# Kernel optimization log

Measured on AMD Instinct MI355X. Metric: run time of the kernel, lower is better.

The kernel has to match this reference:

```python
import jax, jax.numpy as jnp
import numpy as np
import math

B, S, N, D_IN = 32, 60, 25, 100
GRU, TEMB, SEMB, SEM_IN, CH, OUT, NH = 512, 512, 512, 768, 256, 512, 8


def _ln(x, g, b, eps=1e-5):
    m = jnp.mean(x, axis=-1, keepdims=True)
    v = jnp.mean((x - m) ** 2, axis=-1, keepdims=True)
    return (x - m) * jax.lax.rsqrt(v + eps) * g + b


def _gru_dir(x, w_ih, w_hh, b_ih, b_hh, reverse):
    # x: [BN, S, F]; PyTorch GRU gate order (r, z, n); returns final hidden [BN, H]
    H = w_hh.shape[1]
    gi_all = jnp.einsum('bsf,gf->bsg', x, w_ih) + b_ih  # precompute input-side gates

    def step(h, gi):
        gh = h @ w_hh.T + b_hh
        i_r, i_z, i_n = jnp.split(gi, 3, axis=-1)
        h_r, h_z, h_n = jnp.split(gh, 3, axis=-1)
        r = jax.nn.sigmoid(i_r + h_r)
        z = jax.nn.sigmoid(i_z + h_z)
        n = jnp.tanh(i_n + r * h_n)
        h_new = (1.0 - z) * n + z * h
        return h_new, None

    h0 = jnp.zeros((x.shape[0], H), x.dtype)
    h_last, _ = jax.lax.scan(step, h0, jnp.swapaxes(gi_all, 0, 1), reverse=reverse)
    return h_last


def _forward(x, seq1_w1, seq1_b1, seq1_w2, seq1_b2, ln2_g, ln2_b,
             gru_wih_f, gru_whh_f, gru_bih_f, gru_bhh_f,
             gru_wih_b, gru_whh_b, gru_bih_b, gru_bhh_b,
             ln_g, ln_b, attn_in_w, attn_in_b, fc_ta_w, fc_ta_b,
             ln3_g, ln3_b, semantic_embs, sem_w, sem_b, lnsem_g, lnsem_b,
             att_alpha, dist_adj,
             gcn_w0, gcn_b0, gcn_w1, gcn_b1, gcn_w2, gcn_b2,
             gln1_g, gln1_b, gln2_g, gln2_b,
             enc_ln_g, enc_ln_b, fc_w, fc_b):
    Bx, Sx, Nx, _ = x.shape
    # --- latent_correlation_layer ---
    xr = jnp.transpose(x, (0, 2, 1, 3)).reshape(Bx * Nx, Sx, -1)  # [BN,S,D]
    h = jax.nn.relu(xr @ seq1_w1 + seq1_b1)
    h = jax.nn.relu(h @ seq1_w2 + seq1_b2)  # dropout p=0
    h = _ln(h, ln2_g, ln2_b)  # [BN,S,512]
    hf = _gru_dir(h, gru_wih_f, gru_whh_f, gru_bih_f, gru_bhh_f, False)
    hb = _gru_dir(h, gru_wih_b, gru_whh_b, gru_bih_b, gru_bhh_b, True)
    hn = jnp.concatenate([hf, hb], axis=-1).reshape(Bx, Nx, 2 * GRU)
    hn = _ln(hn, ln_g, ln_b)  # [B,N,2*GRU]
    # multihead self-attention weights (averaged over heads, then over batch)
    hd = (2 * GRU) // NH
    qkv = hn @ attn_in_w.T + attn_in_b
    q, k, _v = jnp.split(qkv, 3, axis=-1)
    q = q.reshape(Bx, Nx, NH, hd)
    k = k.reshape(Bx, Nx, NH, hd)
    scores = jnp.einsum('bihd,bjhd->bhij', q, k) / math.sqrt(hd)
    attention = jax.nn.softmax(scores, axis=-1).mean(axis=1).mean(axis=0)  # [N,N]
    # --- node features ---
    wr = jax.nn.relu(hn @ fc_ta_w + fc_ta_b)
    X = _ln(wr, ln3_g, ln3_b)  # [B,N,TEMB]
    te = _ln(semantic_embs @ sem_w + sem_b, lnsem_g, lnsem_b)  # [N,SEMB]
    X = jnp.concatenate([X, jnp.broadcast_to(te, (Bx,) + te.shape)], axis=-1)  # [B,N,TEMB+SEMB]
    # cosine-similarity embedding attention (same for every batch element)
    en = te / jnp.maximum(jnp.linalg.norm(te, axis=-1, keepdims=True), 1e-8)
    embed_att = en @ en.T  # [N,N]
    attention = (att_alpha * dist_adj + (1.0 - att_alpha) * embed_att) * attention
    # case-amplification mask (detached in the original -> stop_gradient)
    m = jax.lax.stop_gradient(attention)
    m = jnp.maximum(m, 0.0) ** 2.5
    m = m / jnp.max(m)
    mask = (m >= 0.08).astype(x.dtype)
    adj = attention * mask
    # --- GCN block (GCNConv, add_self_loops=False, normalize=False, dense adjacency) ---
    def gcn(Xin, W, b):
        # out[i] = sum_j adj[j,i] * (Xin[j] @ W) + b  (source->target flow)
        return jnp.einsum('ji,bjf->bif', adj, Xin @ W) + b
    Xg = jax.nn.relu(gcn(X, gcn_w0, gcn_b0))
    Xg = jax.nn.relu(_ln(gcn(Xg, gcn_w1, gcn_b1) + Xg, gln1_g, gln1_b))
    Xg = jax.nn.relu(_ln(gcn(Xg, gcn_w2, gcn_b2) + Xg, gln2_g, gln2_b))
    # --- encoder head ---
    Xg = _ln(Xg, enc_ln_g, enc_ln_b)
    X_hat = jax.nn.relu(jnp.concatenate([X, Xg], axis=-1) @ fc_w + fc_b)  # [B,N,OUT]
    return X_hat


def setup_inputs():
    key = jax.random.key(0)
    c = [0]

    def nrm(shape, scale=1.0):
        c[0] += 1
        return (jax.random.normal(jax.random.fold_in(key, c[0]), shape) * scale).astype(jnp.float32)

    z = lambda *s: jnp.zeros(s, jnp.float32)
    o = lambda *s: jnp.ones(s, jnp.float32)
    FDIM = TEMB + SEMB
    d = {
        'x': nrm((B, S, N, D_IN)),
        'seq1_w1': nrm((D_IN, 256), 0.06), 'seq1_b1': z(256),
        'seq1_w2': nrm((256, 512), 0.05), 'seq1_b2': z(512),
        'ln2_g': o(512), 'ln2_b': z(512),
        'gru_wih_f': nrm((3 * GRU, 512), 0.04), 'gru_whh_f': nrm((3 * GRU, GRU), 0.04),
        'gru_bih_f': z(3 * GRU), 'gru_bhh_f': z(3 * GRU),
        'gru_wih_b': nrm((3 * GRU, 512), 0.04), 'gru_whh_b': nrm((3 * GRU, GRU), 0.04),
        'gru_bih_b': z(3 * GRU), 'gru_bhh_b': z(3 * GRU),
        'ln_g': o(2 * GRU), 'ln_b': z(2 * GRU),
        'attn_in_w': nrm((3 * 2 * GRU, 2 * GRU), 0.03), 'attn_in_b': z(3 * 2 * GRU),
        'fc_ta_w': nrm((2 * GRU, TEMB), 0.04), 'fc_ta_b': z(TEMB),
        'ln3_g': o(TEMB), 'ln3_b': z(TEMB),
        'semantic_embs': nrm((N, SEM_IN)),
        'sem_w': nrm((SEM_IN, SEMB), 0.04), 'sem_b': z(SEMB),
        'lnsem_g': o(SEMB), 'lnsem_b': z(SEMB),
        'att_alpha': jnp.float32(0.5),
        'dist_adj': jax.random.uniform(jax.random.fold_in(key, 1000), (N, N), jnp.float32),
        'gcn_w0': nrm((FDIM, CH), 0.04), 'gcn_b0': z(CH),
        'gcn_w1': nrm((CH, CH), 0.06), 'gcn_b1': z(CH),
        'gcn_w2': nrm((CH, CH), 0.06), 'gcn_b2': z(CH),
        'gln1_g': o(CH), 'gln1_b': z(CH),
        'gln2_g': o(CH), 'gln2_b': z(CH),
        'enc_ln_g': o(CH), 'enc_ln_b': z(CH),
        'fc_w': nrm((FDIM + CH, OUT), 0.04), 'fc_b': z(OUT),
    }
    return d


def reference(x, seq1_w1, seq1_b1, seq1_w2, seq1_b2, ln2_g, ln2_b,
              gru_wih_f, gru_whh_f, gru_bih_f, gru_bhh_f,
              gru_wih_b, gru_whh_b, gru_bih_b, gru_bhh_b,
              ln_g, ln_b, attn_in_w, attn_in_b, fc_ta_w, fc_ta_b,
              ln3_g, ln3_b, semantic_embs, sem_w, sem_b, lnsem_g, lnsem_b,
              att_alpha, dist_adj,
              gcn_w0, gcn_b0, gcn_w1, gcn_b1, gcn_w2, gcn_b2,
              gln1_g, gln1_b, gln2_g, gln2_b,
              enc_ln_g, enc_ln_b, fc_w, fc_b):
    return _forward(x, seq1_w1, seq1_b1, seq1_w2, seq1_b2, ln2_g, ln2_b,
                    gru_wih_f, gru_whh_f, gru_bih_f, gru_bhh_f,
                    gru_wih_b, gru_whh_b, gru_bih_b, gru_bhh_b,
                    ln_g, ln_b, attn_in_w, attn_in_b, fc_ta_w, fc_ta_b,
                    ln3_g, ln3_b, semantic_embs, sem_w, sem_b, lnsem_g, lnsem_b,
                    att_alpha, dist_adj,
                    gcn_w0, gcn_b0, gcn_w1, gcn_b1, gcn_w2, gcn_b2,
                    gln1_g, gln1_b, gln2_g, gln2_b,
                    enc_ln_g, enc_ln_b, fc_w, fc_b)
```

## Files before the change

kernel.cpp:

```cpp
#include <hip/hip_runtime.h>
#include <hip/hip_bf16.h>
#include <math.h>

#define BB 32
#define SS 60
#define NN_ 25
#define DIN 100
#define BN 800
#define GRU_H 512
#define FDIM 1024
#define CH 256
#define OUTD 512

typedef unsigned short ushort_t;
typedef unsigned int u32;
typedef unsigned long long u64;
typedef float f32x4 __attribute__((ext_vector_type(4)));
typedef __bf16 bf16x8 __attribute__((ext_vector_type(8)));
typedef short s16x8 __attribute__((ext_vector_type(8)));

static const size_t O_HSEQB = 0;
static const size_t O_WB    = 12288000;
static const size_t O_HF32  = 13860864;
static const size_t O_HRING = 14680064;
static const size_t O_HN    = 15908864;
static const size_t O_QKV   = 16728064;
static const size_t O_SC    = 18366464;
static const size_t O_ADJ   = 18530304;
static const size_t O_WR    = 18530944;
static const size_t O_TEP   = 18940544;
static const size_t O_TE    = 18953344;
static const size_t O_XCAT  = 18966144;
static const size_t O_GTMP  = 19990144;
static const size_t O_XG0   = 20194944;
static const size_t O_XG1   = 20399744;
static const size_t O_XG2   = 20604544;
static const size_t O_W1TB  = 20809344;
static const size_t O_W2TB  = 20825728;
static const size_t O_AWB   = 20891264;
static const size_t O_FTWB  = 21939840;
static const size_t O_SMWB  = 22201984;
static const size_t O_G0WB  = 22398592;
static const size_t O_G1WB  = 22529664;
static const size_t O_G2WB  = 22562432;
static const size_t O_FCWB  = 22595200;
static const size_t O_FLAGS = 22922880;

__device__ __forceinline__ ushort_t f2b(float v)
{
  __hip_bfloat16 b = __float2bfloat16(v);
  return *reinterpret_cast<ushort_t*>(&b);
}

__device__ __forceinline__ float sig_fast(float v)
{
  return 1.f / (1.f + __expf(-v));
}
__device__ __forceinline__ float tanh_fast(float v)
{
  return 1.f - 2.f / (1.f + __expf(2.f * v));
}

__device__ __forceinline__ void block_reduce2(float& s, float& q, float* scratch)
{
  __syncthreads();
  #pragma unroll
  for (int off = 32; off > 0; off >>= 1) {
    s += __shfl_down(s, off);
    q += __shfl_down(q, off);
  }
  int tid = threadIdx.x;
  int w = tid >> 6;
  if ((tid & 63) == 0) { scratch[w * 2] = s; scratch[w * 2 + 1] = q; }
  __syncthreads();
  if (tid == 0) {
    float ss = 0.f, qq = 0.f;
    int nw = blockDim.x >> 6;
    for (int i = 0; i < nw; i++) { ss += scratch[i * 2]; qq += scratch[i * 2 + 1]; }
    scratch[0] = ss; scratch[1] = qq;
  }
  __syncthreads();
  s = scratch[0]; q = scratch[1];
}

__global__ __launch_bounds__(256) void k_cvt_plain_all(
    const float* __restrict__ wih_f, const float* __restrict__ whh_f,
    const float* __restrict__ wih_b, const float* __restrict__ whh_b,
    const float* __restrict__ attn_w,
    ushort_t* __restrict__ wb, ushort_t* __restrict__ awb)
{
  int i = blockIdx.x * 256 + threadIdx.x;
  wb[i]           = f2b(wih_f[i]);
  wb[786432 + i]  = f2b(whh_f[i]);
  wb[1572864 + i] = f2b(wih_b[i]);
  wb[2359296 + i] = f2b(whh_b[i]);
  awb[i]          = f2b(attn_w[i]);
  awb[786432 + i] = f2b(attn_w[786432 + i]);
  int j = 1572864 + i;
  if (j < 2097152) awb[j] = f2b(attn_w[j]);
}

struct TJob {
  const float* src; ushort_t* dst;
  int K, N, KP, base;
};

__global__ __launch_bounds__(256) void k_cvt_t_all(
    TJob j0, TJob j1, TJob j2, TJob j3, TJob j4, TJob j5, TJob j6, TJob j7)
{
  __shared__ float tile[32][33];
  int t = blockIdx.x;
  TJob jb = j0;
  if (t >= j7.base) jb = j7;
  else if (t >= j6.base) jb = j6;
  else if (t >= j5.base) jb = j5;
  else if (t >= j4.base) jb = j4;
  else if (t >= j3.base) jb = j3;
  else if (t >= j2.base) jb = j2;
  else if (t >= j1.base) jb = j1;
  int local = t - jb.base;
  int ktiles = (jb.KP + 31) >> 5;
  int n0 = (local / ktiles) * 32;
  int k0 = (local % ktiles) * 32;
  int tx = threadIdx.x & 31, ty = threadIdx.x >> 5;
  #pragma unroll
  for (int i = 0; i < 4; i++) {
    int k = k0 + ty + i * 8, n = n0 + tx;
    tile[ty + i * 8][tx] = (k < jb.K && n < jb.N) ? jb.src[(size_t)k * jb.N + n] : 0.f;
  }
  __syncthreads();
  #pragma unroll
  for (int i = 0; i < 4; i++) {
    int n = n0 + ty + i * 8, k = k0 + tx;
    if (n < jb.N && k < jb.KP) jb.dst[(size_t)n * jb.KP + k] = f2b(tile[tx][ty + i * 8]);
  }
}

__global__ __launch_bounds__(256, 1) void k_mlp_fused(
    const float* __restrict__ x,
    const ushort_t* __restrict__ w1tb,
    const float* __restrict__ b1,
    const ushort_t* __restrict__ w2tb,
    const float* __restrict__ b2,
    const float* __restrict__ g, const float* __restrict__ be,
    ushort_t* __restrict__ hseqb)
{
  __shared__ __align__(16) ushort_t xb[64][136];
  __shared__ __align__(16) ushort_t Bl[512][40];
  __shared__ __align__(16) ushort_t h1[64][264];
  const int tid = threadIdx.x;
  const int r0 = blockIdx.x * 64;

  {
    int rr = tid >> 2;
    int d0 = (tid & 3) * 32;
    int r = r0 + rr;
    int bn = r / SS, s = r % SS;
    int b = bn / NN_, n = bn % NN_;
    const float* xp = x + (((size_t)b * SS + s) * NN_ + n) * DIN;
    ushort_t tmp[32];
    #pragma unroll
    for (int i = 0; i < 32; i++) {
      int d = d0 + i;
      tmp[i] = (d < DIN) ? f2b(xp[d]) : (ushort_t)0;
    }
    #pragma unroll
    for (int i = 0; i < 4; i++)
      *reinterpret_cast<s16x8*>(&xb[rr][d0 + i * 8]) = *reinterpret_cast<s16x8*>(&tmp[i * 8]);
  }
  const int wid = tid >> 6, l = tid & 63, lr = l & 15, lg = l >> 4;
  const int srow = tid >> 2, skg = (tid & 3) * 8;

  f32x4 acc1[16] = {};
  for (int kc = 0; kc < 4; kc++) {
    __syncthreads();
    #pragma unroll
    for (int i = 0; i < 4; i++) {
      int row = srow + i * 64;
      *reinterpret_cast<s16x8*>(&Bl[row][skg]) =
          *reinterpret_cast<const s16x8*>(w1tb + (size_t)row * 128 + kc * 32 + skg);
    }
    __syncthreads();
    bf16x8 aF = *reinterpret_cast<const bf16x8*>(&xb[wid * 16 + lr][kc * 32 + lg * 8]);
    #pragma unroll
    for (int ni = 0; ni < 16; ni++) {
      bf16x8 bF = *reinterpret_cast<const bf16x8*>(&Bl[ni * 16 + lr][lg * 8]);
      acc1[ni] = __builtin_amdgcn_mfma_f32_16x16x32_bf16(aF, bF, acc1[ni], 0, 0, 0);
    }
  }
  #pragma unroll
  for (int ni = 0; ni < 16; ni++) {
    #pragma unroll
    for (int r = 0; r < 4; r++) {
      int row = wid * 16 + lg * 4 + r;
      int col = ni * 16 + lr;
      h1[row][col] = f2b(fmaxf(acc1[ni][r] + b1[col], 0.f));
    }
  }

  f32x4 acc2[32] = {};
  for (int kc = 0; kc < 8; kc++) {
    __syncthreads();
    #pragma unroll
    for (int i = 0; i < 8; i++) {
      int row = srow + i * 64;
      *reinterpret_cast<s16x8*>(&Bl[row][skg]) =
          *reinterpret_cast<const s16x8*>(w2tb + (size_t)row * 256 + kc * 32 + skg);
    }
    __syncthreads();
    bf16x8 aF = *reinterpret_cast<const bf16x8*>(&h1[wid * 16 + lr][kc * 32 + lg * 8]);
    #pragma unroll
    for (int ni = 0; ni < 32; ni++) {
      bf16x8 bF = *reinterpret_cast<const bf16x8*>(&Bl[ni * 16 + lr][lg * 8]);
      acc2[ni] = __builtin_amdgcn_mfma_f32_16x16x32_bf16(aF, bF, acc2[ni], 0, 0, 0);
    }
  }

  float su[4] = {0.f, 0.f, 0.f, 0.f}, sq[4] = {0.f, 0.f, 0.f, 0.f};
  #pragma unroll
  for (int ni = 0; ni < 32; ni++) {
    float bb = b2[ni * 16 + lr];
    #pragma unroll
    for (int r = 0; r < 4; r++) {
      float v = fmaxf(acc2[ni][r] + bb, 0.f);
      acc2[ni][r] = v;
      su[r] += v; sq[r] += v * v;
    }
  }
  #pragma unroll
  for (int off = 1; off < 16; off <<= 1) {
    #pragma unroll
    for (int r = 0; r < 4; r++) {
      su[r] += __shfl_xor(su[r], off);
      sq[r] += __shfl_xor(sq[r], off);
    }
  }
  #pragma unroll
  for (int r = 0; r < 4; r++) {
    float mean = su[r] * (1.f / 512.f);
    float var = sq[r] * (1.f / 512.f) - mean * mean;
    float rs = rsqrtf(var + 1e-5f);
    int rowg = r0 + wid * 16 + lg * 4 + r;
    ushort_t* outp = hseqb + (size_t)rowg * 512;
    #pragma unroll
    for (int ni = 0; ni < 32; ni++) {
      int col = ni * 16 + lr;
      outp[col] = f2b((acc2[ni][r] - mean) * rs * g[col] + be[col]);
    }
  }
}

__global__ __launch_bounds__(256, 1) void k_gru_persist(
    const ushort_t* __restrict__ hseqb, const ushort_t* __restrict__ wb,
    const float* __restrict__ bih_f, const float* __restrict__ bhh_f,
    const float* __restrict__ bih_b, const float* __restrict__ bhh_b,
    float* __restrict__ hf32, ushort_t* __restrict__ hring,
    int* __restrict__ flags)
{
  __shared__ __align__(16) ushort_t Xs[2][64][40];
  __shared__ __align__(16) ushort_t Ws[2][6][64][40];
  __shared__ __align__(16) ushort_t Hs[64][520];
  __shared__ int s_item;
  ushort_t (*hpack)[64] = reinterpret_cast<ushort_t (*)[64]>(&Xs[0][0][0]);

  const int tid = threadIdx.x;

  int* qcnt = flags + 448;
  if (tid == 0) {
    u32 xcc;
    asm volatile("s_getreg_b32 %0, hwreg(HW_REG_XCC_ID)" : "=s"(xcc));
    xcc &= 7u;
    int idx = __hip_atomic_fetch_add(qcnt + xcc, 1, __ATOMIC_RELAXED,
                                     __HIP_MEMORY_SCOPE_AGENT);
    s_item = (idx << 3) | (int)xcc;
  }
  __syncthreads();
  const int xcd = s_item & 7;
  const int idx = s_item >> 3;
  const int x3 = xcd & 3;
  const int dir = xcd >> 2;
  const int nmt = (x3 == 0) ? 4 : 3;
  if (idx >= nmt * 8) return;
  const int mt = (idx >> 3) * 4 + x3;
  const int jt = idx & 7;
  const int j0g = jt * 64;
  const int m0g = mt * 64;
  const int chain = dir * 13 + mt;
  int* flagp = flags + chain * 16;

  const ushort_t* __restrict__ wih = wb + (size_t)dir * 1572864;
  const ushort_t* __restrict__ whh = wih + 786432;
  const float* __restrict__ bih = dir ? bih_b : bih_f;
  const float* __restrict__ bhh = dir ? bhh_b : bhh_f;
  const size_t dirOff = (size_t)dir * 409600;

  const int srow = tid >> 2;
  const int skg = (tid & 3) * 8;
  const int smg = m0g + srow;
  const int smg_c = (smg < BN) ? smg : 0;

  const ushort_t* pw[6];
  #pragma unroll
  for (int tt = 0; tt < 6; tt++) {
    const ushort_t* src = (tt < 3) ? wih : whh;
    int gate = (tt < 3) ? tt : tt - 3;
    int jglob = gate * 512 + j0g + srow;
    pw[tt] = src + (size_t)jglob * 512 + skg;
  }

  const int wid = tid >> 6;
  const int l = tid & 63;
  const int lr = l & 15;
  const int lg = l >> 4;
  const int mbase = (wid >> 1) * 32;
  const int nbase = (wid & 1) * 32;

  float rbr[2], rbz[2], rbin[2], rbhn[2];
  #pragma unroll
  for (int ni = 0; ni < 2; ni++) {
    int j = j0g + nbase + ni * 16 + lr;
    rbr[ni]  = bih[j] + bhh[j];
    rbz[ni]  = bih[512 + j] + bhh[512 + j];
    rbin[ni] = bih[1024 + j];
    rbhn[ni] = bhh[1024 + j];
  }

  float hpreg[2][2][4] = {};

  for (int t = 0; t < SS; ++t) {
    const int xt = dir ? (SS - 1 - t) : t;
    const ushort_t* __restrict__ hprev = hring + (size_t)(t % 3) * 819200 + dirOff;
    ushort_t* __restrict__ hnew = hring + (size_t)((t + 1) % 3) * 819200 + dirOff;
    const ushort_t* __restrict__ px = hseqb + ((size_t)smg_c * SS + xt) * 512 + skg;

    s16x8 rx = *reinterpret_cast<const s16x8*>(px);
    s16x8 rw[6];
    #pragma unroll
    for (int tt = 0; tt < 6; tt++) rw[tt] = *reinterpret_cast<const s16x8*>(pw[tt]);

    if (t > 0 && tid == 0) {
      while (__hip_atomic_load(flagp, __ATOMIC_RELAXED, __HIP_MEMORY_SCOPE_SYSTEM) < 8 * t) {
        __builtin_amdgcn_s_sleep(2);
      }
    }
    __syncthreads();

    {
      const ushort_t* ph = hprev + (size_t)smg_c * 512 + skg;
      u64 hv[32];
      #pragma unroll
      for (int c = 0; c < 16; c++) {
        hv[2 * c]     = *reinterpret_cast<const volatile u64*>(ph + c * 32);
        hv[2 * c + 1] = *reinterpret_cast<const volatile u64*>(ph + c * 32 + 4);
      }
      #pragma unroll
      for (int c = 0; c < 16; c++) {
        *reinterpret_cast<u64*>(&Hs[srow][c * 32 + skg])     = hv[2 * c];
        *reinterpret_cast<u64*>(&Hs[srow][c * 32 + skg + 4]) = hv[2 * c + 1];
      }
    }
    *reinterpret_cast<s16x8*>(&Xs[0][srow][skg]) = rx;
    #pragma unroll
    for (int tt = 0; tt < 6; tt++) *reinterpret_cast<s16x8*>(&Ws[0][tt][srow][skg]) = rw[tt];
    __syncthreads();

    f32x4 accr[2][2] = {};
    f32x4 accz[2][2] = {};
    f32x4 accin[2][2] = {};
    f32x4 acchn[2][2] = {};

    for (int it = 0; it < 16; ++it) {
      const int cur = it & 1;
      if (it < 15) {
        const int k0 = (it + 1) * 32;
        rx = *reinterpret_cast<const s16x8*>(px + k0);
        #pragma unroll
        for (int tt = 0; tt < 6; tt++) rw[tt] = *reinterpret_cast<const s16x8*>(pw[tt] + k0);
      }

      bf16x8 xA[2], hA[2];
      #pragma unroll
      for (int mi = 0; mi < 2; mi++) {
        xA[mi] = *reinterpret_cast<const bf16x8*>(&Xs[cur][mbase + mi * 16 + lr][lg * 8]);
        hA[mi] = *reinterpret_cast<const bf16x8*>(&Hs[mbase + mi * 16 + lr][it * 32 + lg * 8]);
      }
      #pragma unroll
      for (int ni = 0; ni < 2; ni++) {
        const int wrow = nbase + ni * 16 + lr;
        bf16x8 bWr = *reinterpret_cast<const bf16x8*>(&Ws[cur][0][wrow][lg * 8]);
        bf16x8 bWz = *reinterpret_cast<const bf16x8*>(&Ws[cur][1][wrow][lg * 8]);
        bf16x8 bWn = *reinterpret_cast<const bf16x8*>(&Ws[cur][2][wrow][lg * 8]);
        bf16x8 bVr = *reinterpret_cast<const bf16x8*>(&Ws[cur][3][wrow][lg * 8]);
        bf16x8 bVz = *reinterpret_cast<const bf16x8*>(&Ws[cur][4][wrow][lg * 8]);
        bf16x8 bVn = *reinterpret_cast<const bf16x8*>(&Ws[cur][5][wrow][lg * 8]);
        #pragma unroll
        for (int mi = 0; mi < 2; mi++) {
          accr[mi][ni]  = __builtin_amdgcn_mfma_f32_16x16x32_bf16(xA[mi], bWr, accr[mi][ni], 0, 0, 0);
          accr[mi][ni]  = __builtin_amdgcn_mfma_f32_16x16x32_bf16(hA[mi], bVr, accr[mi][ni], 0, 0, 0);
          accz[mi][ni]  = __builtin_amdgcn_mfma_f32_16x16x32_bf16(xA[mi], bWz, accz[mi][ni], 0, 0, 0);
          accz[mi][ni]  = __builtin_amdgcn_mfma_f32_16x16x32_bf16(hA[mi], bVz, accz[mi][ni], 0, 0, 0);
          accin[mi][ni] = __builtin_amdgcn_mfma_f32_16x16x32_bf16(xA[mi], bWn, accin[mi][ni], 0, 0, 0);
          acchn[mi][ni] = __builtin_amdgcn_mfma_f32_16x16x32_bf16(hA[mi], bVn, acchn[mi][ni], 0, 0, 0);
        }
      }

      if (it < 15) {
        const int nxt = cur ^ 1;
        *reinterpret_cast<s16x8*>(&Xs[nxt][srow][skg]) = rx;
        #pragma unroll
        for (int tt = 0; tt < 6; tt++) *reinterpret_cast<s16x8*>(&Ws[nxt][tt][srow][skg]) = rw[tt];
      }
      __syncthreads();
    }

    #pragma unroll
    for (int mi = 0; mi < 2; mi++) {
      #pragma unroll
      for (int ni = 0; ni < 2; ni++) {
        #pragma unroll
        for (int r = 0; r < 4; r++) {
          float sr = accr[mi][ni][r] + rbr[ni];
          float sz = accz[mi][ni][r] + rbz[ni];
          float rg = sig_fast(sr);
          float zg = sig_fast(sz);
          float ng = tanh_fast(accin[mi][ni][r] + rbin[ni] + rg * (acchn[mi][ni][r] + rbhn[ni]));
          hpreg[mi][ni][r] = (1.f - zg) * ng + zg * hpreg[mi][ni][r];
        }
      }
    }

    if (t < SS - 1) {
      #pragma unroll
      for (int mi = 0; mi < 2; mi++)
        #pragma unroll
        for (int ni = 0; ni < 2; ni++)
          #pragma unroll
          for (int r = 0; r < 4; r++)
            hpack[mbase + mi * 16 + lg * 4 + r][nbase + ni * 16 + lr] = f2b(hpreg[mi][ni][r]);
      __syncthreads();
      {
        int row = tid >> 2;
        int gm = m0g + row;
        if (gm < BN) {
          ushort_t* dst = hnew + (size_t)gm * 512 + j0g + (tid & 3) * 16;
          *reinterpret_cast<s16x8*>(dst) =
              *reinterpret_cast<s16x8*>(&hpack[row][(tid & 3) * 16]);
          *reinterpret_cast<s16x8*>(dst + 8) =
              *reinterpret_cast<s16x8*>(&hpack[row][(tid & 3) * 16 + 8]);
        }
      }
      __syncthreads();
      if (tid == 0)
        __hip_atomic_fetch_add(flagp, 1, __ATOMIC_RELAXED, __HIP_MEMORY_SCOPE_SYSTEM);
    } else {
      float* hfin = hf32 + dirOff;
      #pragma unroll
      for (int mi = 0; mi < 2; mi++) {
        #pragma unroll
        for (int r = 0; r < 4; r++) {
          int m = m0g + mbase + mi * 16 + lg * 4 + r;
          if (m >= BN) continue;
          #pragma unroll
          for (int ni = 0; ni < 2; ni++) {
            int j = j0g + nbase + ni * 16 + lr;
            hfin[(size_t)m * 512 + j] = hpreg[mi][ni][r];
          }
        }
      }
    }
  }
}

__global__ __launch_bounds__(256) void k_ln_hn(
    const float* __restrict__ hf, const float* __restrict__ hb,
    const float* __restrict__ g, const float* __restrict__ be,
    float* __restrict__ hn)
{
  __shared__ float scratch[8];
  int row = blockIdx.x, tid = threadIdx.x;
  float v[4];
  float s = 0.f, q = 0.f;
  #pragma unroll
  for (int p = 0; p < 4; p++) {
    int c = p * 256 + tid;
    float val = (c < 512) ? hf[(size_t)row * 512 + c] : hb[(size_t)row * 512 + (c - 512)];
    v[p] = val; s += val; q += val * val;
  }
  block_reduce2(s, q, scratch);
  float mean = s * (1.f / 1024.f);
  float var = q * (1.f / 1024.f) - mean * mean;
  float rs = rsqrtf(var + 1e-5f);
  #pragma unroll
  for (int p = 0; p < 4; p++) {
    int c = p * 256 + tid;
    hn[(size_t)row * 1024 + c] = (v[p] - mean) * rs * g[c] + be[c];
  }
}

template<int ACT>
__global__ __launch_bounds__(256) void k_bgemm(
    const float* __restrict__ A, const ushort_t* __restrict__ B,
    const float* __restrict__ bias, float* __restrict__ C,
    int M, int N, int K, int lda, int ldc)
{
  __shared__ __align__(16) ushort_t Al[64][40];
  __shared__ __align__(16) ushort_t Bl[64][40];
  const int tid = threadIdx.x;
  const int n0g = blockIdx.x * 64, m0g = blockIdx.y * 64;
  const int srow = tid >> 2, skg = (tid & 3) * 8;
  const int smg = (m0g + srow < M) ? (m0g + srow) : (M - 1);
  const int sng = (n0g + srow < N) ? (n0g + srow) : (N - 1);
  const float* pa = A + (size_t)smg * lda + skg;
  const ushort_t* pb = B + (size_t)sng * K + skg;
  const int wid = tid >> 6, l = tid & 63, lr = l & 15, lg = l >> 4;
  const int mbase = (wid >> 1) * 32, nbase = (wid & 1) * 32;
  f32x4 acc[2][2] = {};

  for (int k0 = 0; k0 < K; k0 += 32) {
    float4 a0 = *reinterpret_cast<const float4*>(pa + k0);
    float4 a1 = *reinterpret_cast<const float4*>(pa + k0 + 4);
    s16x8 bv = *reinterpret_cast<const s16x8*>(pb + k0);
    ushort_t tmp[8] = {f2b(a0.x), f2b(a0.y), f2b(a0.z), f2b(a0.w),
                       f2b(a1.x), f2b(a1.y), f2b(a1.z), f2b(a1.w)};
    *reinterpret_cast<s16x8*>(&Al[srow][skg]) = *reinterpret_cast<s16x8*>(tmp);
    *reinterpret_cast<s16x8*>(&Bl[srow][skg]) = bv;
    __syncthreads();
    bf16x8 aF[2], bF[2];
    #pragma unroll
    for (int mi = 0; mi < 2; mi++)
      aF[mi] = *reinterpret_cast<const bf16x8*>(&Al[mbase + mi * 16 + lr][lg * 8]);
    #pragma unroll
    for (int ni = 0; ni < 2; ni++)
      bF[ni] = *reinterpret_cast<const bf16x8*>(&Bl[nbase + ni * 16 + lr][lg * 8]);
    #pragma unroll
    for (int mi = 0; mi < 2; mi++)
      #pragma unroll
      for (int ni = 0; ni < 2; ni++)
        acc[mi][ni] = __builtin_amdgcn_mfma_f32_16x16x32_bf16(aF[mi], bF[ni], acc[mi][ni], 0, 0, 0);
    __syncthreads();
  }
  #pragma unroll
  for (int mi = 0; mi < 2; mi++) {
    #pragma unroll
    for (int r = 0; r < 4; r++) {
      int mg = m0g + mbase + mi * 16 + lg * 4 + r;
      if (mg >= M) continue;
      #pragma unroll
      for (int ni = 0; ni < 2; ni++) {
        int ng = n0g + nbase + ni * 16 + lr;
        if (ng >= N) continue;
        float v = acc[mi][ni][r] + (bias ? bias[ng] : 0.f);
        if (ACT == 1) v = fmaxf(v, 0.f);
        C[(size_t)mg * ldc + ng] = v;
      }
    }
  }
}

__global__ __launch_bounds__(256) void k_scores(const float* __restrict__ qkv,
                                                float* __restrict__ sc)
{
  int b = blockIdx.x, h = blockIdx.y;
  __shared__ float qs[25][128];
  __shared__ float ks[25][129];
  __shared__ float ps[25][26];
  int tid = threadIdx.x;
  for (int idx = tid; idx < 3200; idx += 256) {
    int i = idx >> 7, d = idx & 127;
    const float* base = qkv + (size_t)(b * 25 + i) * 2048 + h * 128 + d;
    qs[i][d] = base[0];
    ks[i][d] = base[1024];
  }
  __syncthreads();
  const float scale = 0.08838834764831845f;
  for (int e = tid; e < 625; e += 256) {
    int i = e / 25, j = e % 25;
    float s = 0.f;
    for (int d = 0; d < 128; d++) s += qs[i][d] * ks[j][d];
    ps[i][j] = s * scale;
  }
  __syncthreads();
  if (tid < 25) {
    float mx = -1e30f;
    for (int j = 0; j < 25; j++) mx = fmaxf(mx, ps[tid][j]);
    float s = 0.f;
    for (int j = 0; j < 25; j++) { float ev = expf(ps[tid][j] - mx); ps[tid][j] = ev; s += ev; }
    float inv = 1.f / s;
    for (int j = 0; j < 25; j++) ps[tid][j] *= inv;
  }
  __syncthreads();
  float* out = sc + (size_t)(b * 8 + h) * 640;
  for (int e = tid; e < 625; e += 256) out[e] = ps[e / 25][e % 25];
}

template<int PER>
__global__ __launch_bounds__(256) void k_ln_rows(
    const float* __restrict__ src, float* __restrict__ dst,
    const float* __restrict__ g, const float* __restrict__ be,
    int dstStride, int dstOff)
{
  __shared__ float scratch[8];
  int row = blockIdx.x, tid = threadIdx.x;
  const int C = PER * 256;
  float v[PER];
  float s = 0.f, q = 0.f;
  #pragma unroll
  for (int p = 0; p < PER; p++) {
    v[p] = src[(size_t)row * C + p * 256 + tid];
    s += v[p]; q += v[p] * v[p];
  }
  block_reduce2(s, q, scratch);
  float mean = s / (float)C;
  float var = q / (float)C - mean * mean;
  float rs = rsqrtf(var + 1e-5f);
  #pragma unroll
  for (int p = 0; p < PER; p++) {
    int c = p * 256 + tid;
    dst[(size_t)row * dstStride + dstOff + c] = (v[p] - mean) * rs * g[c] + be[c];
  }
}

__global__ __launch_bounds__(256) void k_bcast_te(const float* __restrict__ te,
                                                  float* __restrict__ xcat)
{
  int row = blockIdx.x, tid = threadIdx.x;
  int n = row % 25;
  xcat[(size_t)row * 1280 + 512 + tid] = te[n * 512 + tid];
  xcat[(size_t)row * 1280 + 768 + tid] = te[n * 512 + 256 + tid];
}

__global__ __launch_bounds__(1024) void k_adj(
    const float* __restrict__ sc, const float* __restrict__ te,
    const float* __restrict__ alpha_p, const float* __restrict__ dist,
    float* __restrict__ adj)
{
  __shared__ float tes[25][517];
  __shared__ float als[625];
  __shared__ float dots[625];
  __shared__ float scratch[16];
  __shared__ float mxs;
  int tid = threadIdx.x;

  for (int idx = tid; idx < 12800; idx += 1024)
    tes[idx >> 9][idx & 511] = te[idx];
  __syncthreads();

  if (tid < 625) {
    int i = tid / 25, j = tid % 25;
    float s = 0.f;
    for (int gq = 0; gq < 256; gq++) s += sc[(size_t)gq * 640 + tid];
    als[tid] = s * (1.f / 256.f);
    float dt = 0.f;
    const float* ti = tes[i];
    const float* tj = tes[j];
    for (int d = 0; d < 512; d++) dt += ti[d] * tj[d];
    dots[tid] = dt;
  }
  __syncthreads();
  float alpha = alpha_p[0];
  float lm = 0.f;
  if (tid < 625) {
    int i = tid / 25, j = tid % 25;
    float ni = 1.f / fmaxf(sqrtf(dots[i * 26]), 1e-8f);
    float nj = 1.f / fmaxf(sqrtf(dots[j * 26]), 1e-8f);
    float emb = dots[tid] * ni * nj;
    float a = (alpha * dist[tid] + (1.f - alpha) * emb) * als[tid];
    als[tid] = a;
    lm = powf(fmaxf(a, 0.f), 2.5f);
  }
  #pragma unroll
  for (int off = 32; off > 0; off >>= 1) lm = fmaxf(lm, __shfl_down(lm, off));
  int w = tid >> 6;
  if ((tid & 63) == 0) scratch[w] = lm;
  __syncthreads();
  if (tid == 0) {
    float m2 = scratch[0];
    for (int i = 1; i < 16; i++) m2 = fmaxf(m2, scratch[i]);
    mxs = m2;
  }
  __syncthreads();
  if (tid < 625) {
    float a = als[tid];
    float m = powf(fmaxf(a, 0.f), 2.5f) / mxs;
    adj[tid] = (m >= 0.08f) ? a : 0.f;
  }
}

template<int RESID, int LNORM>
__global__ __launch_bounds__(256) void k_mix(
    const float* __restrict__ adj, const float* __restrict__ tmp,
    const float* __restrict__ bias, const float* __restrict__ resid,
    const float* __restrict__ g, const float* __restrict__ be,
    float* __restrict__ out)
{
  __shared__ float adjs[25];
  __shared__ float scratch[8];
  int row = blockIdx.x;
  int b = row / 25, i = row % 25;
  int f = threadIdx.x;
  if (f < 25) adjs[f] = adj[f * 25 + i];
  __syncthreads();
  float acc = bias[f];
  const float* tp = tmp + (size_t)b * 25 * 256 + f;
  #pragma unroll 5
  for (int j = 0; j < 25; j++) acc += adjs[j] * tp[(size_t)j * 256];
  if (RESID) acc += resid[(size_t)row * 256 + f];
  float v = acc;
  if (LNORM) {
    float s = v, q = v * v;
    block_reduce2(s, q, scratch);
    float mean = s * (1.f / 256.f);
    float var = q * (1.f / 256.f) - mean * mean;
    v = (v - mean) * rsqrtf(var + 1e-5f) * g[f] + be[f];
  }
  out[(size_t)row * 256 + f] = fmaxf(v, 0.f);
}

extern "C" void kernel_launch(void* const* d_in, const int* in_sizes, int n_in,
                              void* d_out, int out_size, void* d_ws, size_t ws_size,
                              hipStream_t stream)
{
  (void)in_sizes; (void)n_in; (void)out_size; (void)ws_size;

  const float* x         = (const float*)d_in[0];
  const float* seq1_w1   = (const float*)d_in[1];
  const float* seq1_b1   = (const float*)d_in[2];
  const float* seq1_w2   = (const float*)d_in[3];
  const float* seq1_b2   = (const float*)d_in[4];
  const float* ln2_g     = (const float*)d_in[5];
  const float* ln2_b     = (const float*)d_in[6];
  const float* gru_wih_f = (const float*)d_in[7];
  const float* gru_whh_f = (const float*)d_in[8];
  const float* gru_bih_f = (const float*)d_in[9];
  const float* gru_bhh_f = (const float*)d_in[10];
  const float* gru_wih_b = (const float*)d_in[11];
  const float* gru_whh_b = (const float*)d_in[12];
  const float* gru_bih_b = (const float*)d_in[13];
  const float* gru_bhh_b = (const float*)d_in[14];
  const float* ln_g      = (const float*)d_in[15];
  const float* ln_b      = (const float*)d_in[16];
  const float* attn_in_w = (const float*)d_in[17];
  const float* attn_in_b = (const float*)d_in[18];
  const float* fc_ta_w   = (const float*)d_in[19];
  const float* fc_ta_b   = (const float*)d_in[20];
  const float* ln3_g     = (const float*)d_in[21];
  const float* ln3_b     = (const float*)d_in[22];
  const float* sem_embs  = (const float*)d_in[23];
  const float* sem_w     = (const float*)d_in[24];
  const float* sem_b     = (const float*)d_in[25];
  const float* lnsem_g   = (const float*)d_in[26];
  const float* lnsem_b   = (const float*)d_in[27];
  const float* att_alpha = (const float*)d_in[28];
  const float* dist_adj  = (const float*)d_in[29];
  const float* gcn_w0    = (const float*)d_in[30];
  const float* gcn_b0    = (const float*)d_in[31];
  const float* gcn_w1    = (const float*)d_in[32];
  const float* gcn_b1    = (const float*)d_in[33];
  const float* gcn_w2    = (const float*)d_in[34];
  const float* gcn_b2    = (const float*)d_in[35];
  const float* gln1_g    = (const float*)d_in[36];
  const float* gln1_b    = (const float*)d_in[37];
  const float* gln2_g    = (const float*)d_in[38];
  const float* gln2_b    = (const float*)d_in[39];
  const float* enc_ln_g  = (const float*)d_in[40];
  const float* enc_ln_b  = (const float*)d_in[41];
  const float* fc_w      = (const float*)d_in[42];
  const float* fc_b      = (const float*)d_in[43];

  float* w = (float*)d_ws;
  ushort_t* hseqb = (ushort_t*)(w + O_HSEQB);
  ushort_t* wb    = (ushort_t*)(w + O_WB);
  float* hf32 = w + O_HF32;
  ushort_t* hring = (ushort_t*)(w + O_HRING);
  float* hn   = w + O_HN;
  float* qkv  = w + O_QKV;
  float* sc   = w + O_SC;
  float* adjw = w + O_ADJ;
  float* wr   = w + O_WR;
  float* tep  = w + O_TEP;
  float* te   = w + O_TE;
  float* xcat = w + O_XCAT;
  float* gtmp = w + O_GTMP;
  float* xg0  = w + O_XG0;
  float* xg1  = w + O_XG1;
  float* xg2  = w + O_XG2;
  ushort_t* w1tb = (ushort_t*)(w + O_W1TB);
  ushort_t* w2tb = (ushort_t*)(w + O_W2TB);
  ushort_t* awb  = (ushort_t*)(w + O_AWB);
  ushort_t* ftwb = (ushort_t*)(w + O_FTWB);
  ushort_t* smwb = (ushort_t*)(w + O_SMWB);
  ushort_t* g0wb = (ushort_t*)(w + O_G0WB);
  ushort_t* g1wb = (ushort_t*)(w + O_G1WB);
  ushort_t* g2wb = (ushort_t*)(w + O_G2WB);
  ushort_t* fcwb = (ushort_t*)(w + O_FCWB);
  int* flags = (int*)(w + O_FLAGS);

  hipMemsetAsync(hring, 0, (size_t)819200 * sizeof(ushort_t), stream);
  hipMemsetAsync(flags, 0, 512 * sizeof(int), stream);

  k_cvt_plain_all<<<3072, 256, 0, stream>>>(gru_wih_f, gru_whh_f, gru_wih_b,
                                            gru_whh_b, attn_in_w, wb, awb);
  {
    TJob j0 = {seq1_w1, w1tb, 100, 256, 128, 0};
    TJob j1 = {seq1_w2, w2tb, 256, 512, 256, 32};
    TJob j2 = {fc_ta_w, ftwb, 1024, 512, 1024, 160};
    TJob j3 = {sem_w, smwb, 768, 512, 768, 672};
    TJob j4 = {gcn_w0, g0wb, 1024, 256, 1024, 1056};
    TJob j5 = {gcn_w1, g1wb, 256, 256, 256, 1312};
    TJob j6 = {gcn_w2, g2wb, 256, 256, 256, 1376};
    TJob j7 = {fc_w, fcwb, 1280, 512, 1280, 1440};
    k_cvt_t_all<<<2080, 256, 0, stream>>>(j0, j1, j2, j3, j4, j5, j6, j7);
  }

  k_mlp_fused<<<750, 256, 0, stream>>>(x, w1tb, seq1_b1, w2tb, seq1_b2,
                                       ln2_g, ln2_b, hseqb);

  k_gru_persist<<<256, 256, 0, stream>>>(
      hseqb, wb, gru_bih_f, gru_bhh_f, gru_bih_b, gru_bhh_b, hf32, hring, flags);

  k_ln_hn<<<800, 256, 0, stream>>>(hf32, hf32 + 409600, ln_g, ln_b, hn);

  k_bgemm<0><<<dim3(32, 13), 256, 0, stream>>>(
      hn, awb, attn_in_b, qkv, 800, 2048, 1024, 1024, 2048);

  k_scores<<<dim3(32, 8), 256, 0, stream>>>(qkv, sc);

  k_bgemm<0><<<dim3(8, 1), 256, 0, stream>>>(
      sem_embs, smwb, sem_b, tep, 25, 512, 768, 768, 512);
  k_ln_rows<2><<<25, 256, 0, stream>>>(tep, te, lnsem_g, lnsem_b, 512, 0);

  k_bgemm<1><<<dim3(8, 13), 256, 0, stream>>>(
      hn, ftwb, fc_ta_b, wr, 800, 512, 1024, 1024, 512);
  k_ln_rows<2><<<800, 256, 0, stream>>>(wr, xcat, ln3_g, ln3_b, 1280, 0);
  k_bcast_te<<<800, 256, 0, stream>>>(te, xcat);

  k_adj<<<1, 1024, 0, stream>>>(sc, te, att_alpha, dist_adj, adjw);

  k_bgemm<0><<<dim3(4, 13), 256, 0, stream>>>(
      xcat, g0wb, nullptr, gtmp, 800, 256, 1024, 1280, 256);
  k_mix<0, 0><<<800, 256, 0, stream>>>(adjw, gtmp, gcn_b0, nullptr, nullptr, nullptr, xg0);
  k_bgemm<0><<<dim3(4, 13), 256, 0, stream>>>(
      xg0, g1wb, nullptr, gtmp, 800, 256, 256, 256, 256);
  k_mix<1, 1><<<800, 256, 0, stream>>>(adjw, gtmp, gcn_b1, xg0, gln1_g, gln1_b, xg1);
  k_bgemm<0><<<dim3(4, 13), 256, 0, stream>>>(
      xg1, g2wb, nullptr, gtmp, 800, 256, 256, 256, 256);
  k_mix<1, 1><<<800, 256, 0, stream>>>(adjw, gtmp, gcn_b2, xg1, gln2_g, gln2_b, xg2);

  k_ln_rows<1><<<800, 256, 0, stream>>>(xg2, xcat, enc_ln_g, enc_ln_b, 1280, 1024);

  k_bgemm<1><<<dim3(8, 13), 256, 0, stream>>>(
      xcat, fcwb, fc_b, (float*)d_out, 800, 512, 1280, 1280, 512);
}
```

Measured before the change: 1.580 ms.

## Stream GRU weights directly into MFMA registers and stage full X tile per step

The persistent GRU kernel no longer double-buffers weight and input K-slices through shared memory with a barrier per K-chunk. Each wave now owns a 16-column slice of the gates and loads its weight fragments straight from global (L2) into MFMA operands. The full 64x512 X and H tiles are staged into LDS once per timestep, so the inner K loop runs without any __syncthreads. The cost is reloading weights from global every timestep, more registers for 4x4 accumulators, and larger LDS use.

```diff
diff --git a/kernel.cpp b/kernel.cpp
--- a/kernel.cpp
+++ b/kernel.cpp
@@ -257,11 +257,10 @@
     float* __restrict__ hf32, ushort_t* __restrict__ hring,
     int* __restrict__ flags)
 {
-  __shared__ __align__(16) ushort_t Xs[2][64][40];
-  __shared__ __align__(16) ushort_t Ws[2][6][64][40];
-  __shared__ __align__(16) ushort_t Hs[64][520];
+  __shared__ __align__(16) ushort_t Xf[64][520];
+  __shared__ __align__(16) ushort_t Hf[64][520];
+  __shared__ __align__(16) ushort_t hpack[64][72];
   __shared__ int s_item;
-  ushort_t (*hpack)[64] = reinterpret_cast<ushort_t (*)[64]>(&Xs[0][0][0]);
 
   const int tid = threadIdx.x;
 
@@ -295,37 +294,30 @@
   const size_t dirOff = (size_t)dir * 409600;
 
   const int srow = tid >> 2;
-  const int skg = (tid & 3) * 8;
-  const int smg = m0g + srow;
+  const int skg  = (tid & 3) * 8;
+  const int smg  = m0g + srow;
   const int smg_c = (smg < BN) ? smg : 0;
-
-  const ushort_t* pw[6];
-  #pragma unroll
-  for (int tt = 0; tt < 6; tt++) {
-    const ushort_t* src = (tt < 3) ? wih : whh;
-    int gate = (tt < 3) ? tt : tt - 3;
-    int jglob = gate * 512 + j0g + srow;
-    pw[tt] = src + (size_t)jglob * 512 + skg;
-  }
 
   const int wid = tid >> 6;
   const int l = tid & 63;
   const int lr = l & 15;
   const int lg = l >> 4;
-  const int mbase = (wid >> 1) * 32;
-  const int nbase = (wid & 1) * 32;
-
-  float rbr[2], rbz[2], rbin[2], rbhn[2];
-  #pragma unroll
-  for (int ni = 0; ni < 2; ni++) {
-    int j = j0g + nbase + ni * 16 + lr;
-    rbr[ni]  = bih[j] + bhh[j];
-    rbz[ni]  = bih[512 + j] + bhh[512 + j];
-    rbin[ni] = bih[1024 + j];
-    rbhn[ni] = bhh[1024 + j];
-  }
-
-  float hpreg[2][2][4] = {};
+  const int jg = j0g + (wid << 4) + lr;
+
+  const ushort_t* pwf[6];
+  #pragma unroll
+  for (int tt = 0; tt < 6; tt++) {
+    const ushort_t* src = (tt < 3) ? wih : whh;
+    int gate = (tt < 3) ? tt : tt - 3;
+    pwf[tt] = src + ((size_t)(gate * 512 + jg) * 512) + lg * 8;
+  }
+
+  const float rbr  = bih[jg] + bhh[jg];
+  const float rbz  = bih[512 + jg] + bhh[512 + jg];
+  const float rbin = bih[1024 + jg];
+  const float rbhn = bhh[1024 + jg];
+
+  float hpreg[4][4] = {};
 
   for (int t = 0; t < SS; ++t) {
     const int xt = dir ? (SS - 1 - t) : t;
@@ -333,10 +325,10 @@
     ushort_t* __restrict__ hnew = hring + (size_t)((t + 1) % 3) * 819200 + dirOff;
     const ushort_t* __restrict__ px = hseqb + ((size_t)smg_c * SS + xt) * 512 + skg;
 
-    s16x8 rx = *reinterpret_cast<const s16x8*>(px);
-    s16x8 rw[6];
-    #pragma unroll
-    for (int tt = 0; tt < 6; tt++) rw[tt] = *reinterpret_cast<const s16x8*>(pw[tt]);
+    s16x8 rxv[16];
+    #pragma unroll
+    for (int c = 0; c < 16; c++)
+      rxv[c] = *reinterpret_cast<const s16x8*>(px + c * 32);
 
     if (t > 0 && tid == 0) {
       while (__hip_atomic_load(flagp, __ATOMIC_RELAXED, __HIP_MEMORY_SCOPE_SYSTEM) < 8 * t) {
@@ -355,88 +347,61 @@
       }
       #pragma unroll
       for (int c = 0; c < 16; c++) {
-        *reinterpret_cast<u64*>(&Hs[srow][c * 32 + skg])     = hv[2 * c];
-        *reinterpret_cast<u64*>(&Hs[srow][c * 32 + skg + 4]) = hv[2 * c + 1];
+        *reinterpret_cast<s16x8*>(&Xf[srow][c * 32 + skg]) = rxv[c];
+        *reinterpret_cast<u64*>(&Hf[srow][c * 32 + skg])     = hv[2 * c];
+        *reinterpret_cast<u64*>(&Hf[srow][c * 32 + skg + 4]) = hv[2 * c + 1];
       }
     }
-    *reinterpret_cast<s16x8*>(&Xs[0][srow][skg]) = rx;
-    #pragma unroll
-    for (int tt = 0; tt < 6; tt++) *reinterpret_cast<s16x8*>(&Ws[0][tt][srow][skg]) = rw[tt];
     __syncthreads();
 
-    f32x4 accr[2][2] = {};
-    f32x4 accz[2][2] = {};
-    f32x4 accin[2][2] = {};
-    f32x4 acchn[2][2] = {};
-
+    f32x4 accr[4] = {};
+    f32x4 accz[4] = {};
+    f32x4 accin[4] = {};
+    f32x4 acchn[4] = {};
+
+    #pragma unroll 4
     for (int it = 0; it < 16; ++it) {
-      const int cur = it & 1;
-      if (it < 15) {
-        const int k0 = (it + 1) * 32;
-        rx = *reinterpret_cast<const s16x8*>(px + k0);
+      const int k0 = it * 32;
+      bf16x8 bW[6];
+      #pragma unroll
+      for (int tt = 0; tt < 6; tt++)
+        bW[tt] = *reinterpret_cast<const bf16x8*>(pwf[tt] + k0);
+      bf16x8 xA[4], hA[4];
+      #pragma unroll
+      for (int mi = 0; mi < 4; mi++) {
+        xA[mi] = *reinterpret_cast<const bf16x8*>(&Xf[mi * 16 + lr][k0 + lg * 8]);
+        hA[mi] = *reinterpret_cast<const bf16x8*>(&Hf[mi * 16 + lr][k0 + lg * 8]);
+      }
+      #pragma unroll
+      for (int mi = 0; mi < 4; mi++) {
+        accr[mi]  = __builtin_amdgcn_mfma_f32_16x16x32_bf16(xA[mi], bW[0], accr[mi], 0, 0, 0);
+        accr[mi]  = __builtin_amdgcn_mfma_f32_16x16x32_bf16(hA[mi], bW[3], accr[mi], 0, 0, 0);
+        accz[mi]  = __builtin_amdgcn_mfma_f32_16x16x32_bf16(xA[mi], bW[1], accz[mi], 0, 0, 0);
+        accz[mi]  = __builtin_amdgcn_mfma_f32_16x16x32_bf16(hA[mi], bW[4], accz[mi], 0, 0, 0);
+        accin[mi] = __builtin_amdgcn_mfma_f32_16x16x32_bf16(xA[mi], bW[2], accin[mi], 0, 0, 0);
+        acchn[mi] = __builtin_amdgcn_mfma_f32_16x16x32_bf16(hA[mi], bW[5], acchn[mi], 0, 0, 0);
+      }
+    }
+
+    #pragma unroll
+    for (int mi = 0; mi < 4; mi++) {
+      #pragma unroll
+      for (int r = 0; r < 4; r++) {
+        float sr = accr[mi][r] + rbr;
+        float sz = accz[mi][r] + rbz;
+        float rg = sig_fast(sr);
+        float zg = sig_fast(sz);
+        float ng = tanh_fast(accin[mi][r] + rbin + rg * (acchn[mi][r] + rbhn));
+        hpreg[mi][r] = (1.f - zg) * ng + zg * hpreg[mi][r];
+      }
+    }
+
+    if (t < SS - 1) {
+      #pragma unroll
+      for (int mi = 0; mi < 4; mi++)
         #pragma unroll
-        for (int tt = 0; tt < 6; tt++) rw[tt] = *reinterpret_cast<const s16x8*>(pw[tt] + k0);
-      }
-
-      bf16x8 xA[2], hA[2];
-      #pragma unroll
-      for (int mi = 0; mi < 2; mi++) {
-        xA[mi] = *reinterpret_cast<const bf16x8*>(&Xs[cur][mbase + mi * 16 + lr][lg * 8]);
-        hA[mi] = *reinterpret_cast<const bf16x8*>(&Hs[mbase + mi * 16 + lr][it * 32 + lg * 8]);
-      }
-      #pragma unroll
-      for (int ni = 0; ni < 2; ni++) {
-        const int wrow = nbase + ni * 16 + lr;
-        bf16x8 bWr = *reinterpret_cast<const bf16x8*>(&Ws[cur][0][wrow][lg * 8]);
-        bf16x8 bWz = *reinterpret_cast<const bf16x8*>(&Ws[cur][1][wrow][lg * 8]);
-        bf16x8 bWn = *reinterpret_cast<const bf16x8*>(&Ws[cur][2][wrow][lg * 8]);
-        bf16x8 bVr = *reinterpret_cast<const bf16x8*>(&Ws[cur][3][wrow][lg * 8]);
-        bf16x8 bVz = *reinterpret_cast<const bf16x8*>(&Ws[cur][4][wrow][lg * 8]);
-        bf16x8 bVn = *reinterpret_cast<const bf16x8*>(&Ws[cur][5][wrow][lg * 8]);
-        #pragma unroll
-        for (int mi = 0; mi < 2; mi++) {
-          accr[mi][ni]  = __builtin_amdgcn_mfma_f32_16x16x32_bf16(xA[mi], bWr, accr[mi][ni], 0, 0, 0);
-          accr[mi][ni]  = __builtin_amdgcn_mfma_f32_16x16x32_bf16(hA[mi], bVr, accr[mi][ni], 0, 0, 0);
-          accz[mi][ni]  = __builtin_amdgcn_mfma_f32_16x16x32_bf16(xA[mi], bWz, accz[mi][ni], 0, 0, 0);
-          accz[mi][ni]  = __builtin_amdgcn_mfma_f32_16x16x32_bf16(hA[mi], bVz, accz[mi][ni], 0, 0, 0);
-          accin[mi][ni] = __builtin_amdgcn_mfma_f32_16x16x32_bf16(xA[mi], bWn, accin[mi][ni], 0, 0, 0);
-          acchn[mi][ni] = __builtin_amdgcn_mfma_f32_16x16x32_bf16(hA[mi], bVn, acchn[mi][ni], 0, 0, 0);
-        }
-      }
-
-      if (it < 15) {
-        const int nxt = cur ^ 1;
-        *reinterpret_cast<s16x8*>(&Xs[nxt][srow][skg]) = rx;
-        #pragma unroll
-        for (int tt = 0; tt < 6; tt++) *reinterpret_cast<s16x8*>(&Ws[nxt][tt][srow][skg]) = rw[tt];
-      }
-      __syncthreads();
-    }
-
-    #pragma unroll
-    for (int mi = 0; mi < 2; mi++) {
-      #pragma unroll
-      for (int ni = 0; ni < 2; ni++) {
-        #pragma unroll
-        for (int r = 0; r < 4; r++) {
-          float sr = accr[mi][ni][r] + rbr[ni];
-          float sz = accz[mi][ni][r] + rbz[ni];
-          float rg = sig_fast(sr);
-          float zg = sig_fast(sz);
-          float ng = tanh_fast(accin[mi][ni][r] + rbin[ni] + rg * (acchn[mi][ni][r] + rbhn[ni]));
-          hpreg[mi][ni][r] = (1.f - zg) * ng + zg * hpreg[mi][ni][r];
-        }
-      }
-    }
-
-    if (t < SS - 1) {
-      #pragma unroll
-      for (int mi = 0; mi < 2; mi++)
-        #pragma unroll
-        for (int ni = 0; ni < 2; ni++)
-          #pragma unroll
-          for (int r = 0; r < 4; r++)
-            hpack[mbase + mi * 16 + lg * 4 + r][nbase + ni * 16 + lr] = f2b(hpreg[mi][ni][r]);
+        for (int r = 0; r < 4; r++)
+          hpack[mi * 16 + lg * 4 + r][(wid << 4) + lr] = f2b(hpreg[mi][r]);
       __syncthreads();
       {
         int row = tid >> 2;
@@ -455,16 +420,11 @@
     } else {
       float* hfin = hf32 + dirOff;
       #pragma unroll
-      for (int mi = 0; mi < 2; mi++) {
+      for (int mi = 0; mi < 4; mi++) {
         #pragma unroll
         for (int r = 0; r < 4; r++) {
-          int m = m0g + mbase + mi * 16 + lg * 4 + r;
-          if (m >= BN) continue;
-          #pragma unroll
-          for (int ni = 0; ni < 2; ni++) {
-            int j = j0g + nbase + ni * 16 + lr;
-            hfin[(size_t)m * 512 + j] = hpreg[mi][ni][r];
-          }
+          int m = m0g + mi * 16 + lg * 4 + r;
+          if (m < BN) hfin[(size_t)m * 512 + jg] = hpreg[mi][r];
         }
       }
     }
```

Result: faster. 1.454 ms (-8.0%).
